# Performance work log

Measured on AMD Instinct MI355X. Metric: run time of the kernel, lower is better.

Reference implementation:

```python
import jax, jax.numpy as jnp
import numpy as np

K, D = 1024, 256


def setup_inputs() -> dict:
    key = jax.random.key(0)
    k1, k2 = jax.random.split(key)
    z_e = jax.random.normal(k1, (32, D, 32, 32), dtype=jnp.float32)
    # torch init: uniform_(-1/K, 1/K)
    emb_weight = jax.random.uniform(k2, (K, D), minval=-1.0 / K, maxval=1.0 / K, dtype=jnp.float32)
    return {"z_e": z_e, "emb_weight": emb_weight}


def reference(z_e, emb_weight):
    B, C, W, H = z_e.shape
    # [B, W, H, C] -> flatten to [N, C]
    z = jnp.transpose(z_e, (0, 2, 3, 1))
    z_flat = z.reshape(-1, C)
    # squared euclidean distances; argmin is identical to argmin of cdist
    d2 = (
        jnp.sum(z_flat * z_flat, axis=1, keepdims=True)
        - 2.0 * (z_flat @ emb_weight.T)
        + jnp.sum(emb_weight * emb_weight, axis=1)
    )  # [N, K]
    indices = jnp.argmin(d2, axis=1)  # [N]
    z_q = emb_weight[indices].reshape(B, W, H, C)
    # straight-through: forward value equals z_q, gradient passes to z_e
    z_q_st = z + jax.lax.stop_gradient(z_q - z)
    z_q_out = jnp.transpose(z_q, (0, 3, 1, 2))
    z_q_st_out = jnp.transpose(z_q_st, (0, 3, 1, 2))
    return (z_q_st_out, z_q_out, indices.reshape(B, W * H))
```

## Files before the change

kernel.cpp:

```cpp
#include <hip/hip_runtime.h>
#include <cfloat>
#include <cstdint>

#define THRESH 1.25e-4f

typedef __attribute__((ext_vector_type(8))) _Float16 half8;
typedef __attribute__((ext_vector_type(8))) unsigned short upk8;
typedef __attribute__((ext_vector_type(4))) float facc4;

__device__ __forceinline__ unsigned short f2h(float x) {
  _Float16 h = (_Float16)x;
  return __builtin_bit_cast(unsigned short, h);
}


__global__ __launch_bounds__(256) void precompute_kernel(
    const float* __restrict__ emb, float* __restrict__ Csq,
    unsigned short* __restrict__ ehT, int* __restrict__ flagCount) {
  int blk = blockIdx.x, t = threadIdx.x;
  if (blk < 4) {
    int k = blk * 256 + t;
    const float4* e4 = (const float4*)(emb + ((size_t)k << 8));
    double acc = 0.0;
    for (int d4 = 0; d4 < 64; ++d4) {
      float4 e = e4[d4];
      acc += (double)(e.x * e.x) + (double)(e.y * e.y) +
             (double)(e.z * e.z) + (double)(e.w * e.w);
    }
    Csq[k] = (float)acc;
    if (blk == 0 && t == 0) *flagCount = 0;
  } else {
    int linear = (blk - 4) * 256 + t;
    int code = linear & 1023, kg = linear >> 10;
    const float* ep = emb + ((size_t)code << 8) + (kg << 3);
    float4 e0 = *(const float4*)ep;
    float4 e1 = *(const float4*)(ep + 4);
    upk8 pk;
    pk[0] = f2h(e0.x); pk[1] = f2h(e0.y); pk[2] = f2h(e0.z); pk[3] = f2h(e0.w);
    pk[4] = f2h(e1.x); pk[5] = f2h(e1.y); pk[6] = f2h(e1.z); pk[7] = f2h(e1.w);
    *(upk8*)(ehT + ((size_t)linear << 3)) = pk;
  }
}

__device__ __forceinline__ void stage_half(
    const unsigned short* __restrict__ ehT, char* buf, int h, int t) {
  int w6 = t & 0x1C0;
#pragma unroll
  for (int i = 0; i < 8; ++i) {
    int slot = (i << 9) + t;
    int kg = slot >> 7, cl = slot & 127;
    const unsigned short* g = ehT + (((size_t)(kg << 10) + (h << 7) + cl) << 3);
    char* lp = buf + (((i << 9) + w6) << 4);
    __builtin_amdgcn_global_load_lds(
        (const __attribute__((address_space(1))) unsigned int*)g,
        (__attribute__((address_space(3))) unsigned int*)lp, 16, 0, 0);
  }
}

__global__ __launch_bounds__(512, 2) void phase1_kernel(
    const float* __restrict__ z, const unsigned short* __restrict__ ehT,
    const float* __restrict__ Csq, float* __restrict__ A,
    int* __restrict__ idxbuf, int* __restrict__ flagCount,
    int* __restrict__ flagList) {
  __shared__ char bufA[65536] __attribute__((aligned(16)));
  __shared__ char bufB[65536] __attribute__((aligned(16)));
  __shared__ float Cs[1024];
  __shared__ float mm1[2][4][32], mm2[2][4][32];
  __shared__ int mbi[2][4][32];

  int t = threadIdx.x;
  int n0 = blockIdx.x << 7;
  int b = n0 >> 10, wh0 = n0 & 1023;
  int w = t >> 6, l = t & 63;
  int wv = w & 3, wn = w >> 2;
  int lx = l & 15, lg = l >> 4;

  stage_half(ehT, bufA, 0, t);
  stage_half(ehT, bufB, 1, t);
  ((float2*)Cs)[t] = ((const float2*)Csq)[t];

  half8 afr[2][8];
  double nacc[2] = {0.0, 0.0};
  const float* zb = z + (((size_t)(b * 256)) << 10) + wh0 + wv * 32 + lx;
#pragma unroll
  for (int mi = 0; mi < 2; ++mi) {
#pragma unroll
    for (int kk = 0; kk < 8; ++kk) {
      upk8 pk;
#pragma unroll
      for (int j = 0; j < 8; ++j) {
        int c = kk * 32 + lg * 8 + j;
        float x = zb[((size_t)c << 10) + mi * 16];
        nacc[mi] += (double)(x * x);
        pk[j] = f2h(-2.0f * x);
      }
      afr[mi][kk] = __builtin_bit_cast(half8, pk);
    }
  }
#pragma unroll
  for (int mi = 0; mi < 2; ++mi) {
    double s = nacc[mi];
    s += __shfl_xor(s, 16);
    s += __shfl_xor(s, 32);
    if (wn == 0 && lg == 0) A[n0 + wv * 32 + mi * 16 + lx] = (float)s;
  }
  __syncthreads();

  float m1[8], m2[8];
  int bi[8];
#pragma unroll
  for (int s8 = 0; s8 < 8; ++s8) { m1[s8] = FLT_MAX; m2[s8] = FLT_MAX; bi[s8] = 0; }

#pragma unroll
  for (int h = 0; h < 8; ++h) {
    const char* buf = (h & 1) ? bufB : bufA;
    facc4 acc[2][4];
#pragma unroll
    for (int mi = 0; mi < 2; ++mi)
#pragma unroll
      for (int nj = 0; nj < 4; ++nj) {
        facc4 zf = {0.0f, 0.0f, 0.0f, 0.0f};
        acc[mi][nj] = zf;
      }
#pragma unroll
    for (int kk = 0; kk < 8; ++kk) {
      const char* base = buf + (((((kk << 2) + lg) << 7) + (wn << 6) + lx) << 4);
#pragma unroll
      for (int nj = 0; nj < 4; ++nj) {
        half8 bv = *(const half8*)(base + (nj << 8));
        acc[0][nj] = __builtin_amdgcn_mfma_f32_16x16x32_f16(afr[0][kk], bv, acc[0][nj], 0, 0, 0);
        acc[1][nj] = __builtin_amdgcn_mfma_f32_16x16x32_f16(afr[1][kk], bv, acc[1][nj], 0, 0, 0);
      }
    }
    int cbase = (h << 7) + (wn << 6);
#pragma unroll
    for (int nj = 0; nj < 4; ++nj) {
      float csv = Cs[cbase + nj * 16 + lx];
      int code = cbase + nj * 16 + lx;
#pragma unroll
      for (int mi = 0; mi < 2; ++mi)
#pragma unroll
        for (int reg = 0; reg < 4; ++reg) {
          int s8 = mi * 4 + reg;
          float sv = acc[mi][nj][reg] + csv;
          float hi = fmaxf(sv, m1[s8]);
          bool lt = sv < m1[s8];
          m1[s8] = lt ? sv : m1[s8];
          bi[s8] = lt ? code : bi[s8];
          m2[s8] = fminf(m2[s8], hi);
        }
    }
    if (h < 7) {
      asm volatile("s_waitcnt lgkmcnt(0)" ::: "memory");
      __builtin_amdgcn_s_barrier();
      if (h + 2 < 8) {
        stage_half(ehT, (h & 1) ? bufB : bufA, h + 2, t);
        asm volatile("s_waitcnt vmcnt(8)" ::: "memory");
      } else {
        asm volatile("s_waitcnt vmcnt(0)" ::: "memory");
      }
      __builtin_amdgcn_s_barrier();
    }
  }

#pragma unroll
  for (int s8 = 0; s8 < 8; ++s8) {
    float M1 = m1[s8], M2 = m2[s8];
    int BI = bi[s8];
    for (int off = 8; off > 0; off >>= 1) {
      float om1 = __shfl_xor(M1, off, 16);
      float om2 = __shfl_xor(M2, off, 16);
      int obi = __shfl_xor(BI, off, 16);
      float lo = fminf(M2, om2);
      bool take = (om1 < M1) || (om1 == M1 && obi < BI);
      float loser = take ? M1 : om1;
      M2 = fminf(lo, loser);
      if (take) { M1 = om1; BI = obi; }
    }
    if (lx == 0) {
      int row = ((s8 >> 2) << 4) + (lg << 2) + (s8 & 3);
      mm1[wn][wv][row] = M1; mm2[wn][wv][row] = M2; mbi[wn][wv][row] = BI;
    }
  }
  __syncthreads();
  if (wn == 0 && lx == 0) {
#pragma unroll
    for (int s8 = 0; s8 < 8; ++s8) {
      int row = ((s8 >> 2) << 4) + (lg << 2) + (s8 & 3);
      float a1v = mm1[0][wv][row], a2v = mm2[0][wv][row];
      int ab = mbi[0][wv][row];
      float b1v = mm1[1][wv][row], b2v = mm2[1][wv][row];
      int bb = mbi[1][wv][row];
      bool tb = (b1v < a1v) || (b1v == a1v && bb < ab);
      float M1 = tb ? b1v : a1v;
      int BI = tb ? bb : ab;
      float M2 = fminf(fminf(a2v, b2v), tb ? a1v : b1v);
      int n = n0 + wv * 32 + row;
      idxbuf[n] = BI;
      if (M2 - M1 < THRESH) {
        int pos = atomicAdd(flagCount, 1);
        flagList[pos] = n;
      }
    }
  }
}

__global__ __launch_bounds__(256) void phase2_kernel(
    const float* __restrict__ z, const float* __restrict__ emb,
    const float* __restrict__ Csq, const float* __restrict__ A,
    int* __restrict__ idxbuf, const int* __restrict__ flagCount,
    const int* __restrict__ flagList) {
  __shared__ float zq[4][260];
  __shared__ float Anv[4];
  __shared__ int nn[4];
  __shared__ float sq[4][4];
  __shared__ int sk[4][4];
  int t = threadIdx.x;
  int w = t >> 6, l = t & 63;
  int cnt = *flagCount;
  int nit = (cnt + 3) >> 2;
  for (int it = blockIdx.x; it < nit; it += gridDim.x) {
    __syncthreads();
    int base = it << 2;
    int mcnt = min(4, cnt - base);
    if (t < 4) {
      if (t < mcnt) { int n = flagList[base + t]; nn[t] = n; Anv[t] = A[n]; }
      else nn[t] = -1;
    }
    __syncthreads();
#pragma unroll
    for (int v = 0; v < 4; ++v) {
      int n = nn[v];
      if (n >= 0) {
        int bb = n >> 10, wh = n & 1023;
        zq[v][t] = z[(((size_t)(bb * 256 + t)) << 10) + wh];
      }
    }
    __syncthreads();

    float dot[4][4];
#pragma unroll
    for (int r = 0; r < 4; ++r)
#pragma unroll
      for (int v = 0; v < 4; ++v) dot[r][v] = 0.0f;

    const float4* e0 = (const float4*)(emb + ((size_t)(t + 0) << 8));
    const float4* e1 = (const float4*)(emb + ((size_t)(t + 256) << 8));
    const float4* e2 = (const float4*)(emb + ((size_t)(t + 512) << 8));
    const float4* e3 = (const float4*)(emb + ((size_t)(t + 768) << 8));
#pragma unroll 8
    for (int d4 = 0; d4 < 64; ++d4) {
      float4 ea = e0[d4], eb = e1[d4], ec = e2[d4], ed = e3[d4];
#pragma unroll
      for (int v = 0; v < 4; ++v) {
        float4 zv = *(const float4*)&zq[v][d4 * 4];
        dot[0][v] += zv.x * ea.x + zv.y * ea.y + zv.z * ea.z + zv.w * ea.w;
        dot[1][v] += zv.x * eb.x + zv.y * eb.y + zv.z * eb.z + zv.w * eb.w;
        dot[2][v] += zv.x * ec.x + zv.y * ec.y + zv.z * ec.z + zv.w * ec.w;
        dot[3][v] += zv.x * ed.x + zv.y * ed.y + zv.z * ed.z + zv.w * ed.w;
      }
    }

    float bq[4];
    int bk[4];
#pragma unroll
    for (int v = 0; v < 4; ++v) { bq[v] = FLT_MAX; bk[v] = 0; }
#pragma unroll
    for (int r = 0; r < 4; ++r) {
      int k = t + (r << 8);
      float Ck = Csq[k];
#pragma unroll
      for (int v = 0; v < 4; ++v) {
        float qv = (Anv[v] - 2.0f * dot[r][v]) + Ck;
        if (qv < bq[v]) { bq[v] = qv; bk[v] = k; }
      }
    }

#pragma unroll
    for (int v = 0; v < 4; ++v) {
      float q = bq[v];
      int kk = bk[v];
      for (int off = 32; off > 0; off >>= 1) {
        float oq = __shfl_xor(q, off);
        int ok = __shfl_xor(kk, off);
        if (oq < q || (oq == q && ok < kk)) { q = oq; kk = ok; }
      }
      if (l == 0) { sq[v][w] = q; sk[v][w] = kk; }
    }
    __syncthreads();
    if (t < mcnt) {
      float q = sq[t][0];
      int kk = sk[t][0];
#pragma unroll
      for (int j = 1; j < 4; ++j) {
        float oq = sq[t][j];
        int ok = sk[t][j];
        if (oq < q || (oq == q && ok < kk)) { q = oq; kk = ok; }
      }
      idxbuf[nn[t]] = kk;
    }
  }
}

__global__ __launch_bounds__(256) void gather_kernel(
    const float* __restrict__ emb, const int* __restrict__ idxbuf,
    float* __restrict__ out) {
  __shared__ int sidx[32];
  __shared__ float se[256][34];
  int tid = threadIdx.x;
  int blk = blockIdx.x;
  int n0 = blk * 32;
  int b = n0 >> 10, wh0 = n0 & 1023;
  float* out0 = out;
  float* out1 = out + 8388608;
  float* out2 = out + 16777216;
  if (tid < 32) {
    int ix = idxbuf[n0 + tid];
    sidx[tid] = ix;
    out2[n0 + tid] = (float)ix;
  }
  __syncthreads();
  {
    int v = tid >> 3, d8 = tid & 7;
    int row = sidx[v];
    const float4* e4 = (const float4*)(emb + ((size_t)row << 8));
    for (int it = 0; it < 8; ++it) {
      int d4 = it * 8 + d8;
      float4 e = e4[d4];
      se[d4 * 4 + 0][v] = e.x; se[d4 * 4 + 1][v] = e.y;
      se[d4 * 4 + 2][v] = e.z; se[d4 * 4 + 3][v] = e.w;
    }
  }
  __syncthreads();
  {
    int v = tid & 31, cg = tid >> 5;
    for (int c = cg; c < 256; c += 8) {
      float val = se[c][v];
      size_t o = (((size_t)(b * 256 + c)) << 10) + wh0 + v;
      out0[o] = val;
      out1[o] = val;
    }
  }
}

extern "C" void kernel_launch(void* const* d_in, const int* in_sizes, int n_in,
                              void* d_out, int out_size, void* d_ws, size_t ws_size,
                              hipStream_t stream) {
  const float* z = (const float*)d_in[0];
  const float* emb = (const float*)d_in[1];
  float* ws = (float*)d_ws;
  float* Csq = ws;
  float* A = ws + 1024;
  int* idxbuf = (int*)(ws + 33792);
  int* flagCount = (int*)(ws + 66560);
  int* flagList = (int*)(ws + 66576);
  unsigned short* ehT = (unsigned short*)(ws + 99344);

  precompute_kernel<<<132, 256, 0, stream>>>(emb, Csq, ehT, flagCount);
  phase1_kernel<<<256, 512, 0, stream>>>(z, ehT, Csq, A, idxbuf, flagCount, flagList);
  phase2_kernel<<<1024, 256, 0, stream>>>(z, emb, Csq, A, idxbuf, flagCount, flagList);
  gather_kernel<<<1024, 256, 0, stream>>>(emb, idxbuf, (float*)d_out);
}
```

Measured before the change: 124.3 us.

## Shrink phase1 tile to 64 rows, split codebook across four wave groups

Phase1 now processes 64 rows per block instead of 128, with waves arranged 2 along rows and 4 along codes. The codebook is streamed in 16 quarter-chunks of 32KB into a double buffer instead of 8 chunks of 64KB. The final cross-wave argmin merge now combines four partials. This halves LDS per block and doubles the grid to 512 blocks, aiming at better occupancy and CU fill. In exchange each block loads the full fp16 codebook for half as many rows, doubling global/L2 traffic for it, and takes more barrier steps with less MFMA work per step.

```diff
diff --git a/kernel.cpp b/kernel.cpp
--- a/kernel.cpp
+++ b/kernel.cpp
@@ -42,14 +42,14 @@
   }
 }
 
-__device__ __forceinline__ void stage_half(
-    const unsigned short* __restrict__ ehT, char* buf, int h, int t) {
+__device__ __forceinline__ void stage_q(
+    const unsigned short* __restrict__ ehT, char* buf, int q, int t) {
   int w6 = t & 0x1C0;
 #pragma unroll
-  for (int i = 0; i < 8; ++i) {
+  for (int i = 0; i < 4; ++i) {
     int slot = (i << 9) + t;
-    int kg = slot >> 7, cl = slot & 127;
-    const unsigned short* g = ehT + (((size_t)(kg << 10) + (h << 7) + cl) << 3);
+    int kg = slot >> 6, cl = slot & 63;
+    const unsigned short* g = ehT + (((size_t)(kg << 10) + (q << 6) + cl) << 3);
     char* lp = buf + (((i << 9) + w6) << 4);
     __builtin_amdgcn_global_load_lds(
         (const __attribute__((address_space(1))) unsigned int*)g,
@@ -62,21 +62,21 @@
     const float* __restrict__ Csq, float* __restrict__ A,
     int* __restrict__ idxbuf, int* __restrict__ flagCount,
     int* __restrict__ flagList) {
-  __shared__ char bufA[65536] __attribute__((aligned(16)));
-  __shared__ char bufB[65536] __attribute__((aligned(16)));
+  __shared__ char bufA[32768] __attribute__((aligned(16)));
+  __shared__ char bufB[32768] __attribute__((aligned(16)));
   __shared__ float Cs[1024];
-  __shared__ float mm1[2][4][32], mm2[2][4][32];
-  __shared__ int mbi[2][4][32];
+  __shared__ float mm1[4][2][32], mm2[4][2][32];
+  __shared__ int mbi[4][2][32];
 
   int t = threadIdx.x;
-  int n0 = blockIdx.x << 7;
+  int n0 = blockIdx.x << 6;
   int b = n0 >> 10, wh0 = n0 & 1023;
   int w = t >> 6, l = t & 63;
-  int wv = w & 3, wn = w >> 2;
+  int wv = w & 1, wn = w >> 1;
   int lx = l & 15, lg = l >> 4;
 
-  stage_half(ehT, bufA, 0, t);
-  stage_half(ehT, bufB, 1, t);
+  stage_q(ehT, bufA, 0, t);
+  stage_q(ehT, bufB, 1, t);
   ((float2*)Cs)[t] = ((const float2*)Csq)[t];
 
   half8 afr[2][8];
@@ -111,51 +111,43 @@
 #pragma unroll
   for (int s8 = 0; s8 < 8; ++s8) { m1[s8] = FLT_MAX; m2[s8] = FLT_MAX; bi[s8] = 0; }
 
-#pragma unroll
-  for (int h = 0; h < 8; ++h) {
-    const char* buf = (h & 1) ? bufB : bufA;
-    facc4 acc[2][4];
+#pragma unroll 1
+  for (int q = 0; q < 16; ++q) {
+    const char* buf = (q & 1) ? bufB : bufA;
+    facc4 acc[2];
+#pragma unroll
+    for (int mi = 0; mi < 2; ++mi) {
+      facc4 zf = {0.0f, 0.0f, 0.0f, 0.0f};
+      acc[mi] = zf;
+    }
+#pragma unroll
+    for (int kk = 0; kk < 8; ++kk) {
+      const char* base = buf + (((((kk << 2) + lg) << 6) + (wn << 4) + lx) << 4);
+      half8 bv = *(const half8*)base;
+      acc[0] = __builtin_amdgcn_mfma_f32_16x16x32_f16(afr[0][kk], bv, acc[0], 0, 0, 0);
+      acc[1] = __builtin_amdgcn_mfma_f32_16x16x32_f16(afr[1][kk], bv, acc[1], 0, 0, 0);
+    }
+    int cbase = (q << 6) + (wn << 4);
+    float csv = Cs[cbase + lx];
+    int code = cbase + lx;
 #pragma unroll
     for (int mi = 0; mi < 2; ++mi)
 #pragma unroll
-      for (int nj = 0; nj < 4; ++nj) {
-        facc4 zf = {0.0f, 0.0f, 0.0f, 0.0f};
-        acc[mi][nj] = zf;
-      }
-#pragma unroll
-    for (int kk = 0; kk < 8; ++kk) {
-      const char* base = buf + (((((kk << 2) + lg) << 7) + (wn << 6) + lx) << 4);
-#pragma unroll
-      for (int nj = 0; nj < 4; ++nj) {
-        half8 bv = *(const half8*)(base + (nj << 8));
-        acc[0][nj] = __builtin_amdgcn_mfma_f32_16x16x32_f16(afr[0][kk], bv, acc[0][nj], 0, 0, 0);
-        acc[1][nj] = __builtin_amdgcn_mfma_f32_16x16x32_f16(afr[1][kk], bv, acc[1][nj], 0, 0, 0);
-      }
-    }
-    int cbase = (h << 7) + (wn << 6);
-#pragma unroll
-    for (int nj = 0; nj < 4; ++nj) {
-      float csv = Cs[cbase + nj * 16 + lx];
-      int code = cbase + nj * 16 + lx;
-#pragma unroll
-      for (int mi = 0; mi < 2; ++mi)
-#pragma unroll
-        for (int reg = 0; reg < 4; ++reg) {
-          int s8 = mi * 4 + reg;
-          float sv = acc[mi][nj][reg] + csv;
-          float hi = fmaxf(sv, m1[s8]);
-          bool lt = sv < m1[s8];
-          m1[s8] = lt ? sv : m1[s8];
-          bi[s8] = lt ? code : bi[s8];
-          m2[s8] = fminf(m2[s8], hi);
-        }
-    }
-    if (h < 7) {
+      for (int reg = 0; reg < 4; ++reg) {
+        int s8 = mi * 4 + reg;
+        float sv = acc[mi][reg] + csv;
+        float hi = fmaxf(sv, m1[s8]);
+        bool lt = sv < m1[s8];
+        m1[s8] = lt ? sv : m1[s8];
+        bi[s8] = lt ? code : bi[s8];
+        m2[s8] = fminf(m2[s8], hi);
+      }
+    if (q < 15) {
       asm volatile("s_waitcnt lgkmcnt(0)" ::: "memory");
       __builtin_amdgcn_s_barrier();
-      if (h + 2 < 8) {
-        stage_half(ehT, (h & 1) ? bufB : bufA, h + 2, t);
-        asm volatile("s_waitcnt vmcnt(8)" ::: "memory");
+      if (q < 14) {
+        stage_q(ehT, (q & 1) ? bufB : bufA, q + 2, t);
+        asm volatile("s_waitcnt vmcnt(4)" ::: "memory");
       } else {
         asm volatile("s_waitcnt vmcnt(0)" ::: "memory");
       }
@@ -187,14 +179,17 @@
 #pragma unroll
     for (int s8 = 0; s8 < 8; ++s8) {
       int row = ((s8 >> 2) << 4) + (lg << 2) + (s8 & 3);
-      float a1v = mm1[0][wv][row], a2v = mm2[0][wv][row];
-      int ab = mbi[0][wv][row];
-      float b1v = mm1[1][wv][row], b2v = mm2[1][wv][row];
-      int bb = mbi[1][wv][row];
-      bool tb = (b1v < a1v) || (b1v == a1v && bb < ab);
-      float M1 = tb ? b1v : a1v;
-      int BI = tb ? bb : ab;
-      float M2 = fminf(fminf(a2v, b2v), tb ? a1v : b1v);
+      float M1 = mm1[0][wv][row], M2 = mm2[0][wv][row];
+      int BI = mbi[0][wv][row];
+#pragma unroll
+      for (int j = 1; j < 4; ++j) {
+        float b1 = mm1[j][wv][row], b2 = mm2[j][wv][row];
+        int bb = mbi[j][wv][row];
+        bool tb = (b1 < M1) || (b1 == M1 && bb < BI);
+        float loser = tb ? M1 : b1;
+        M2 = fminf(fminf(M2, b2), loser);
+        if (tb) { M1 = b1; BI = bb; }
+      }
       int n = n0 + wv * 32 + row;
       idxbuf[n] = BI;
       if (M2 - M1 < THRESH) {
@@ -357,7 +352,7 @@
   unsigned short* ehT = (unsigned short*)(ws + 99344);
 
   precompute_kernel<<<132, 256, 0, stream>>>(emb, Csq, ehT, flagCount);
-  phase1_kernel<<<256, 512, 0, stream>>>(z, ehT, Csq, A, idxbuf, flagCount, flagList);
+  phase1_kernel<<<512, 512, 0, stream>>>(z, ehT, Csq, A, idxbuf, flagCount, flagList);
   phase2_kernel<<<1024, 256, 0, stream>>>(z, emb, Csq, A, idxbuf, flagCount, flagList);
   gather_kernel<<<1024, 256, 0, stream>>>(emb, idxbuf, (float*)d_out);
 }
```

New measurement: 115.6 us. 1.08x faster.
